# Kernel tuning notes

Hardware: AMD Instinct MI355X
Metric: run time of the kernel (lower is better)

## Reference

```python
import jax, jax.numpy as jnp
import numpy as np
from jax import lax

B, C, H, W = 4, 64, 128, 128
G, K, CO = 8, 3, 64
KK = K * K
MC = G * KK  # mask channels = 72


def _conv3x3(x, w, b):
    # standard 3x3 conv, stride 1, padding 1, NCHW
    y = lax.conv_general_dilated(x, w, (1, 1), ((1, 1), (1, 1)),
                                 dimension_numbers=('NCHW', 'OIHW', 'NCHW'))
    return y + b[None, :, None, None]


def _deform_conv2d(x, offset, mask, w, b):
    """Modulated deformable conv (DCNv2), stride=1, padding=1, dilation=1.
    offset: [B, 2*G*KK, H, W] interpreted as [B, G, KK, 2(dy,dx), H, W] (torchvision layout).
    mask:   [B, G*KK, H, W].
    w: [Co, C/G, K, K], b: [Co].
    """
    Bn, Cn, Hn, Wn = x.shape
    Co, Cg, Kh, Kw = w.shape
    Gn = Cn // Cg
    KKn = Kh * Kw
    Ho, Wo = Hn, Wn  # stride 1, pad 1, k 3

    off = offset.reshape(Bn, Gn, KKn, 2, Ho, Wo)
    dy, dx = off[:, :, :, 0], off[:, :, :, 1]
    m = mask.reshape(Bn, Gn, 1, KKn, Ho, Wo)

    kh = (jnp.arange(KKn) // Kw).astype(x.dtype)  # kernel row index
    kw = (jnp.arange(KKn) % Kw).astype(x.dtype)
    hh = jnp.arange(Ho, dtype=x.dtype)
    ww = jnp.arange(Wo, dtype=x.dtype)
    # sampling positions: h - pad + kh*dil + dy  -> [B,G,KK,Ho,Wo]
    py = hh[None, None, None, :, None] - 1.0 + kh[None, None, :, None, None] + dy
    px = ww[None, None, None, None, :] - 1.0 + kw[None, None, :, None, None] + dx

    y0 = jnp.floor(py); x0 = jnp.floor(px)
    ly = py - y0; lx = px - x0
    y0i = y0.astype(jnp.int32); x0i = x0.astype(jnp.int32)
    y1i = y0i + 1; x1i = x0i + 1

    xg = x.reshape(Bn, Gn, Cg, Hn * Wn)

    def corner(yi, xi, wgt):
        valid = ((yi >= 0) & (yi < Hn) & (xi >= 0) & (xi < Wn)).astype(x.dtype)
        idx = (jnp.clip(yi, 0, Hn - 1) * Wn + jnp.clip(xi, 0, Wn - 1))
        idx = idx.reshape(Bn, Gn, 1, KKn * Ho * Wo)
        v = jnp.take_along_axis(xg, idx, axis=3).reshape(Bn, Gn, Cg, KKn, Ho, Wo)
        return v * (wgt * valid)[:, :, None]

    val = (corner(y0i, x0i, (1.0 - ly) * (1.0 - lx))
           + corner(y0i, x1i, (1.0 - ly) * lx)
           + corner(y1i, x0i, ly * (1.0 - lx))
           + corner(y1i, x1i, ly * lx))
    val = val * m  # modulation

    wr = w.reshape(Gn, Co // Gn, Cg, KKn)
    out = jnp.einsum('bgckhw,gock->bgohw', val, wr).reshape(Bn, Co, Ho, Wo)
    return out + b[None, :, None, None]


def setup_inputs() -> dict:
    key = jax.random.key(0)
    ks = jax.random.split(key, 8)
    f = lambda k, s, sc=1.0: jax.random.normal(k, s, dtype=jnp.float32) * sc
    return {
        'x': f(ks[0], (B, C, H, W)),
        'share_with_feat': f(ks[1], (B, C, H, W)),
        'offset_feat': f(ks[2], (B, C, H, W)),
        # conv_offset_mask: C -> 3*G*KK (zero-init in original; small random here)
        'w_om': f(ks[3], (3 * MC, C, 3, 3), 0.02),
        'b_om': jnp.zeros((3 * MC,), jnp.float32),
        'w_em1': f(ks[4], (C, 2 * C, 3, 3), 0.05),
        'b_em1': jnp.zeros((C,), jnp.float32),
        'w_em2': f(ks[5], (MC, C, 3, 3), 0.05),
        'b_em2': jnp.zeros((MC,), jnp.float32),
        # deform conv weight: [Co, C/G, 3, 3]
        'w_dc': f(ks[6], (CO, C // G, 3, 3), 0.05),
        'b_dc': f(ks[7], (CO,), 0.05),
    }


def reference(x, share_with_feat, offset_feat, w_om, b_om, w_em1, b_em1,
              w_em2, b_em2, w_dc, b_dc):
    om = _conv3x3(offset_feat, w_om, b_om)
    o1, o2, mask_x = jnp.split(om, 3, axis=1)
    offset = jnp.concatenate([o1, o2], axis=1)
    mask_x = jax.nn.sigmoid(mask_x)
    x_deform = _deform_conv2d(x, offset, mask_x, w_dc, b_dc)
    # extra_mask=True branch
    em = _conv3x3(jnp.concatenate([share_with_feat, offset_feat], axis=1), w_em1, b_em1)
    em = jnp.where(em >= 0, em, 0.1 * em)  # LeakyReLU(0.1)
    em = jax.nn.sigmoid(_conv3x3(em, w_em2, b_em2))
    share_deform = _deform_conv2d(share_with_feat, offset, em, w_dc, b_dc)
    return (x_deform, share_deform)
```

## Files before the change

### kernel.cpp

```cpp
#include <hip/hip_runtime.h>
#include <math.h>

#define BB 4
#define CC 64
#define HH 128
#define WW 128
#define GG 8
#define COO 64
#define HWC (HH*WW)

#define DPAD 12
#define DROW 26

typedef float f32x16 __attribute__((ext_vector_type(16)));
typedef __bf16 bf16x8 __attribute__((ext_vector_type(8)));

__device__ __forceinline__ unsigned short bf16_rn(float f) {
    unsigned int u = __float_as_uint(f);
    unsigned int r = (u + 0x7fffu + ((u >> 16) & 1u)) >> 16;
    return (unsigned short)r;
}
__device__ __forceinline__ float b2f(unsigned short u) {
    return __uint_as_float(((unsigned int)u) << 16);
}

__global__ __launch_bounds__(256) void pack_inputs_kernel(
    const float* __restrict__ x, const float* __restrict__ share,
    const float* __restrict__ offf,
    unsigned int* __restrict__ xs, unsigned short* __restrict__ sc16,
    unsigned short* __restrict__ oc16)
{
    __shared__ unsigned short lds[64][66];
    const int b = blockIdx.y;
    const int pix0 = blockIdx.x * 64;
    const int t = threadIdx.x;
    const int p = t & 63, q = t >> 6;
    const int pl = t & 63, cg = t >> 6;

#pragma unroll
    for (int i = 0; i < 16; i++) {
        int c = i * 4 + q;
        size_t idx = ((size_t)b * 64 + c) * HWC + pix0 + p;
        unsigned short sb = bf16_rn(share[idx]);
        lds[c][p] = sb;
        xs[idx] = (unsigned int)bf16_rn(x[idx]) | ((unsigned int)sb << 16);
    }
    __syncthreads();
    {
        unsigned int u[8];
#pragma unroll
        for (int j = 0; j < 8; j++) {
            unsigned int lo = lds[cg * 16 + 2 * j][pl];
            unsigned int hi = lds[cg * 16 + 2 * j + 1][pl];
            u[j] = lo | (hi << 16);
        }
        unsigned int* dst = (unsigned int*)(sc16 + ((size_t)(b * 4 + cg) * HWC + pix0 + pl) * 16);
        *(uint4*)dst = make_uint4(u[0], u[1], u[2], u[3]);
        *(uint4*)(dst + 4) = make_uint4(u[4], u[5], u[6], u[7]);
    }
    __syncthreads();

#pragma unroll
    for (int i = 0; i < 16; i++) {
        int c = i * 4 + q;
        lds[c][p] = bf16_rn(offf[((size_t)b * 64 + c) * HWC + pix0 + p]);
    }
    __syncthreads();
    {
        unsigned int u[8];
#pragma unroll
        for (int j = 0; j < 8; j++) {
            unsigned int lo = lds[cg * 16 + 2 * j][pl];
            unsigned int hi = lds[cg * 16 + 2 * j + 1][pl];
            u[j] = lo | (hi << 16);
        }
        unsigned int* dst = (unsigned int*)(oc16 + ((size_t)(b * 4 + cg) * HWC + pix0 + pl) * 16);
        *(uint4*)dst = make_uint4(u[0], u[1], u[2], u[3]);
        *(uint4*)(dst + 4) = make_uint4(u[4], u[5], u[6], u[7]);
    }
}

__device__ __forceinline__ void pack_w_one(const float* __restrict__ w,
                                           unsigned short* __restrict__ wp,
                                           int Cout, int COP, int CinTot, int idx) {
    int i  = idx & 15;
    int co = (idx >> 4) % COP;
    int t  = idx / (16 * COP);
    int cg = t & 3;
    int kk = (t >> 2) % 9;
    int seg = t / 36;
    int cin = seg * 64 + cg * 16 + i;
    float v = (co < Cout) ? w[((size_t)co * CinTot + cin) * 9 + kk] : 0.f;
    wp[idx] = bf16_rn(v);
}

__global__ void pack_w_all_kernel(const float* __restrict__ w_om, unsigned short* __restrict__ wp_om,
                                  const float* __restrict__ w_em1, unsigned short* __restrict__ wp_em1,
                                  const float* __restrict__ w_em2, unsigned short* __restrict__ wp_em2) {
    int i = blockIdx.x * 256 + threadIdx.x;
    if (i < 129024) {
        pack_w_one(w_om, wp_om, 216, 224, 64, i);
    } else if (i < 129024 + 73728) {
        pack_w_one(w_em1, wp_em1, 64, 64, 128, i - 129024);
    } else if (i < 129024 + 73728 + 55296) {
        pack_w_one(w_em2, wp_em2, 72, 96, 64, i - 129024 - 73728);
    }
}

template<int NSEG, int NT>
__global__ __launch_bounds__(256) void conv_mfma_kernel(
    const unsigned short* __restrict__ in0,
    const unsigned short* __restrict__ in1,
    const unsigned short* __restrict__ wp,
    const float* __restrict__ bias,
    void* __restrict__ out,
    int Cout, int COP, int out_mode, int act)
{
    constexpr int XS = 128 / (NT * 32);
    const int lane = threadIdx.x & 63;
    const int wid  = threadIdx.x >> 6;
    const int l31  = lane & 31;
    const int half = lane >> 5;
    int tmp = blockIdx.x;
    const int xsp = tmp % XS; tmp /= XS;
    const int rb  = tmp % (HH / 4);
    const int b   = tmp / (HH / 4);
    const int r   = rb * 4 + wid;
    const int px0 = xsp * NT * 32;
    const int co0 = blockIdx.y * 32;

    f32x16 acc[NT];
#pragma unroll
    for (int nt = 0; nt < NT; nt++)
#pragma unroll
        for (int rg = 0; rg < 16; rg++) acc[nt][rg] = 0.f;

    bf16x8 bz;
#pragma unroll
    for (int i = 0; i < 8; i++) bz[i] = (__bf16)0.f;

#pragma unroll
    for (int seg = 0; seg < NSEG; seg++) {
        const unsigned short* in = seg ? in1 : in0;
        const unsigned short* inb = in + (size_t)b * 4 * HWC * 16;
#pragma unroll
        for (int kk = 0; kk < 9; kk++) {
            const int rr = r + kk / 3 - 1;
            const bool rv = (unsigned)rr < (unsigned)HH;
            const int rrc = min(max(rr, 0), HH - 1);
            const int dxo = kk % 3 - 1;
#pragma unroll
            for (int cg = 0; cg < 4; cg++) {
                bf16x8 afrag = *(const bf16x8*)(wp +
                    ((size_t)(((seg * 9 + kk) * 4 + cg) * COP + co0 + l31) * 16 + half * 8));
                if (!rv) afrag = bz;
                const size_t plane = ((size_t)cg * HWC + (size_t)rrc * WW) * 16;
#pragma unroll
                for (int nt = 0; nt < NT; nt++) {
                    const int cc = px0 + nt * 32 + l31 + dxo;
                    bf16x8 bfrag = bz;
                    if ((unsigned)cc < (unsigned)WW)
                        bfrag = *(const bf16x8*)(inb + plane + (size_t)cc * 16 + half * 8);
                    acc[nt] = __builtin_amdgcn_mfma_f32_32x32x16_bf16(afrag, bfrag, acc[nt], 0, 0, 0);
                }
            }
        }
    }

#pragma unroll
    for (int nt = 0; nt < NT; nt++) {
#pragma unroll
        for (int rg = 0; rg < 16; rg++) {
            const int row = (rg & 3) + 8 * (rg >> 2) + 4 * half;
            const int co = co0 + row;
            if (co < Cout) {
                float v = acc[nt][rg] + bias[co];
                if (act == 1)      v = (v >= 0.f) ? v : 0.1f * v;
                else if (act == 2) v = 1.f / (1.f + __expf(-v));
                else if (act == 3 && co >= 144) v = 1.f / (1.f + __expf(-v));
                const int pix = r * WW + px0 + nt * 32 + l31;
                if (out_mode == 2)
                    ((unsigned short*)out)[((size_t)b * Cout + co) * HWC + pix] = bf16_rn(v);
                else
                    ((unsigned short*)out)[((size_t)(b * 4 + (co >> 4)) * HWC + pix) * 16 + (co & 15)] = bf16_rn(v);
            }
        }
    }
}

__global__ __launch_bounds__(256) void deform_fused_kernel(
    const unsigned int* __restrict__ xs,
    const unsigned short* __restrict__ om, const unsigned short* __restrict__ em,
    const float* __restrict__ wdc, const float* __restrict__ bdc,
    float* __restrict__ outx, float* __restrict__ outs)
{
    __shared__ __align__(16) unsigned int lds[24 * DROW * DPAD];

    const int bg = blockIdx.x >> 6;
    const int b = bg >> 3, g = bg & 7;
    const int tile = blockIdx.x & 63;
    const int r0 = (tile >> 3) << 4;
    const int c0 = (tile & 7) << 4;
    const int tx = threadIdx.x & 15, ty = threadIdx.x >> 4;
    const int h = r0 + ty, w = c0 + tx;
    const int wr0 = r0 - 4, wc0 = c0 - 4;

    const unsigned int* xsb = xs + ((size_t)b * 64 + g * 8) * HWC;

#pragma unroll
    for (int i = 0; i < 18; i++) {
        unsigned int slot = (unsigned int)threadIdx.x + i * 256u;
        unsigned int sx = slot % 24u;
        unsigned int t2 = slot / 24u;
        unsigned int sy = t2 % 24u;
        unsigned int c  = t2 / 24u;
        int iy = min(max(wr0 + (int)sy, 0), HH - 1);
        int ix = min(max(wc0 + (int)sx, 0), WW - 1);
        lds[(sy * DROW + sx) * DPAD + c] = xsb[(size_t)c * HWC + iy * WW + ix];
    }

    __syncthreads();

    const int pix = h * WW + w;
    const unsigned short* omb = om + (size_t)b * 216 * HWC + pix + (size_t)g * 18 * HWC;
    const unsigned short* mmb = om + (size_t)b * 216 * HWC + pix + (size_t)(144 + g * 9) * HWC;
    const unsigned short* emb = em + (size_t)b * 72 * HWC + pix + (size_t)g * 9 * HWC;

    float accx[8], accs[8];
#pragma unroll
    for (int o = 0; o < 8; o++) { accx[o] = 0.f; accs[o] = 0.f; }

#pragma unroll
    for (int kk = 0; kk < 9; kk++) {
        const float dy = b2f(omb[(size_t)(kk * 2) * HWC]);
        const float dx = b2f(omb[(size_t)(kk * 2 + 1) * HWC]);
        const float m1 = b2f(mmb[(size_t)kk * HWC]);
        const float m2 = b2f(emb[(size_t)kk * HWC]);

        const float py = (float)(h - 1 + kk / 3) + dy;
        const float px = (float)(w - 1 + kk % 3) + dx;
        const float y0f = floorf(py), x0f = floorf(px);
        const float ly = py - y0f, lx = px - x0f;
        const int y0 = (int)y0f, x0 = (int)x0f;
        const int y1 = y0 + 1, x1 = x0 + 1;
        const bool vy0 = (y0 >= 0) && (y0 < HH), vy1 = (y1 >= 0) && (y1 < HH);
        const bool vx0 = (x0 >= 0) && (x0 < WW), vx1 = (x1 >= 0) && (x1 < WW);
        float w00 = (1.f - ly) * (1.f - lx); if (!(vy0 && vx0)) w00 = 0.f;
        float w01 = (1.f - ly) * lx;         if (!(vy0 && vx1)) w01 = 0.f;
        float w10 = ly * (1.f - lx);         if (!(vy1 && vx0)) w10 = 0.f;
        float w11 = ly * lx;                 if (!(vy1 && vx1)) w11 = 0.f;
        const int cy0 = min(max(y0, 0), HH - 1), cy1 = min(max(y1, 0), HH - 1);
        const int cx0 = min(max(x0, 0), WW - 1), cx1 = min(max(x1, 0), WW - 1);

        const int sy0 = cy0 - wr0, sy1 = cy1 - wr0;
        const int sx0 = cx0 - wc0, sx1 = cx1 - wc0;
        const bool inw = (sy0 >= 0) && (sy1 < 24) && (sx0 >= 0) && (sx1 < 24);

        const float* wk = wdc + (size_t)g * 8 * 8 * 9 + kk;

        if (__builtin_expect(inw, 1)) {
            const int p00 = (sy0 * DROW + sx0) * DPAD, p01 = (sy0 * DROW + sx1) * DPAD;
            const int p10 = (sy1 * DROW + sx0) * DPAD, p11 = (sy1 * DROW + sx1) * DPAD;
#pragma unroll
            for (int ch = 0; ch < 2; ch++) {
                uint4 qa = *(const uint4*)(lds + p00 + ch * 4);
                uint4 qb = *(const uint4*)(lds + p01 + ch * 4);
                uint4 qc = *(const uint4*)(lds + p10 + ch * 4);
                uint4 qd = *(const uint4*)(lds + p11 + ch * 4);
                const unsigned int ua[4] = {qa.x, qa.y, qa.z, qa.w};
                const unsigned int ub[4] = {qb.x, qb.y, qb.z, qb.w};
                const unsigned int uc[4] = {qc.x, qc.y, qc.z, qc.w};
                const unsigned int ud[4] = {qd.x, qd.y, qd.z, qd.w};
#pragma unroll
                for (int j = 0; j < 4; j++) {
                    const int c = ch * 4 + j;
                    float x00 = __uint_as_float(ua[j] << 16), s00 = __uint_as_float(ua[j] & 0xffff0000u);
                    float x01 = __uint_as_float(ub[j] << 16), s01 = __uint_as_float(ub[j] & 0xffff0000u);
                    float x10 = __uint_as_float(uc[j] << 16), s10 = __uint_as_float(uc[j] & 0xffff0000u);
                    float x11 = __uint_as_float(ud[j] << 16), s11 = __uint_as_float(ud[j] & 0xffff0000u);
                    float vx = w00 * x00; vx = fmaf(w01, x01, vx); vx = fmaf(w10, x10, vx); vx = fmaf(w11, x11, vx);
                    float vs = w00 * s00; vs = fmaf(w01, s01, vs); vs = fmaf(w10, s10, vs); vs = fmaf(w11, s11, vs);
                    vx *= m1;
                    vs *= m2;
#pragma unroll
                    for (int o = 0; o < 8; o++) {
                        const float wv = wk[(size_t)(o * 8 + c) * 9];
                        accx[o] = fmaf(vx, wv, accx[o]);
                        accs[o] = fmaf(vs, wv, accs[o]);
                    }
                }
            }
        } else {
            const int i00 = cy0 * WW + cx0, i01 = cy0 * WW + cx1;
            const int i10 = cy1 * WW + cx0, i11 = cy1 * WW + cx1;
#pragma unroll
            for (int c = 0; c < 8; c++) {
                const unsigned int* xc = xsb + (size_t)c * HWC;
                unsigned int a = xc[i00], bq = xc[i01], cq = xc[i10], dq = xc[i11];
                float x00 = __uint_as_float(a << 16),  s00 = __uint_as_float(a & 0xffff0000u);
                float x01 = __uint_as_float(bq << 16), s01 = __uint_as_float(bq & 0xffff0000u);
                float x10 = __uint_as_float(cq << 16), s10 = __uint_as_float(cq & 0xffff0000u);
                float x11 = __uint_as_float(dq << 16), s11 = __uint_as_float(dq & 0xffff0000u);
                float vx = w00 * x00; vx = fmaf(w01, x01, vx); vx = fmaf(w10, x10, vx); vx = fmaf(w11, x11, vx);
                float vs = w00 * s00; vs = fmaf(w01, s01, vs); vs = fmaf(w10, s10, vs); vs = fmaf(w11, s11, vs);
                vx *= m1;
                vs *= m2;
#pragma unroll
                for (int o = 0; o < 8; o++) {
                    const float wv = wk[(size_t)(o * 8 + c) * 9];
                    accx[o] = fmaf(vx, wv, accx[o]);
                    accs[o] = fmaf(vs, wv, accs[o]);
                }
            }
        }
    }

#pragma unroll
    for (int o = 0; o < 8; o++) {
        const float bv = bdc[g * 8 + o];
        outx[((size_t)(b * COO + g * 8 + o)) * HWC + pix] = accx[o] + bv;
        outs[((size_t)(b * COO + g * 8 + o)) * HWC + pix] = accs[o] + bv;
    }
}

extern "C" void kernel_launch(void* const* d_in, const int* in_sizes, int n_in,
                              void* d_out, int out_size, void* d_ws, size_t ws_size,
                              hipStream_t stream) {
    const float* x      = (const float*)d_in[0];
    const float* share  = (const float*)d_in[1];
    const float* offf   = (const float*)d_in[2];
    const float* w_om   = (const float*)d_in[3];
    const float* b_om   = (const float*)d_in[4];
    const float* w_em1  = (const float*)d_in[5];
    const float* b_em1  = (const float*)d_in[6];
    const float* w_em2  = (const float*)d_in[7];
    const float* b_em2  = (const float*)d_in[8];
    const float* w_dc   = (const float*)d_in[9];
    const float* b_dc   = (const float*)d_in[10];

    unsigned int* xs = (unsigned int*)d_ws;
    unsigned short* us = (unsigned short*)(xs + 4194304);
    unsigned short* sc16   = us;
    unsigned short* oc16   = sc16 + 4194304;
    unsigned short* emm    = oc16 + 4194304;
    unsigned short* om_b   = emm + 4194304;
    unsigned short* em_b   = om_b + 14155776;
    unsigned short* wp_om  = em_b + 4718592;
    unsigned short* wp_em1 = wp_om + 129024;
    unsigned short* wp_em2 = wp_em1 + 73728;

    float* outx = (float*)d_out;
    float* outs = outx + 4194304;

    dim3 blk(256);

    pack_inputs_kernel<<<dim3(HWC / 64, BB), blk, 0, stream>>>(x, share, offf, xs, sc16, oc16);
    pack_w_all_kernel<<<(258048 + 255) / 256, blk, 0, stream>>>(
        w_om, wp_om, w_em1, wp_em1, w_em2, wp_em2);

    conv_mfma_kernel<1, 2><<<dim3(BB * (HH / 4) * 2, 7), blk, 0, stream>>>(
        oc16, nullptr, wp_om, b_om, om_b, 216, 224, 2, 3);
    conv_mfma_kernel<2, 1><<<dim3(BB * (HH / 4) * 4, 2), blk, 0, stream>>>(
        sc16, oc16, wp_em1, b_em1, emm, 64, 64, 3, 1);
    conv_mfma_kernel<1, 1><<<dim3(BB * (HH / 4) * 4, 3), blk, 0, stream>>>(
        emm, nullptr, wp_em2, b_em2, em_b, 72, 96, 2, 2);

    deform_fused_kernel<<<dim3(BB * GG * 64), blk, 0, stream>>>(
        xs, om_b, em_b, w_dc, b_dc, outx, outs);
}
```

Before: 276.6 us.

## Stage conv input halo tiles in LDS and tile multiple output-channel blocks per wave

The MFMA 3x3 conv kernel now cooperatively loads a 4-row-plus-halo, 66-pixel input tile for all channel groups into shared memory, then reads B fragments from LDS for every kernel tap, where before each fragment came from global memory. Each wave also computes MREP 32-channel output blocks, so every B fragment feeds several MFMAs. Weight packing pads the output channels to 256/128 to match the new blocking. This cuts redundant global loads of the input, in exchange for extra padded work on the om/em2 convs, shared-memory use, and a barrier between segments.

```diff
diff --git a/kernel.cpp b/kernel.cpp
--- a/kernel.cpp
+++ b/kernel.cpp
@@ -98,91 +98,118 @@
                                   const float* __restrict__ w_em1, unsigned short* __restrict__ wp_em1,
                                   const float* __restrict__ w_em2, unsigned short* __restrict__ wp_em2) {
     int i = blockIdx.x * 256 + threadIdx.x;
-    if (i < 129024) {
-        pack_w_one(w_om, wp_om, 216, 224, 64, i);
-    } else if (i < 129024 + 73728) {
-        pack_w_one(w_em1, wp_em1, 64, 64, 128, i - 129024);
-    } else if (i < 129024 + 73728 + 55296) {
-        pack_w_one(w_em2, wp_em2, 72, 96, 64, i - 129024 - 73728);
-    }
-}
-
-template<int NSEG, int NT>
+    if (i < 147456) {
+        pack_w_one(w_om, wp_om, 216, 256, 64, i);
+    } else if (i < 147456 + 73728) {
+        pack_w_one(w_em1, wp_em1, 64, 64, 128, i - 147456);
+    } else if (i < 147456 + 73728 + 73728) {
+        pack_w_one(w_em2, wp_em2, 72, 128, 64, i - 147456 - 73728);
+    }
+}
+
+template<int NSEG, int MREP, int COP>
 __global__ __launch_bounds__(256) void conv_mfma_kernel(
     const unsigned short* __restrict__ in0,
     const unsigned short* __restrict__ in1,
     const unsigned short* __restrict__ wp,
     const float* __restrict__ bias,
     void* __restrict__ out,
-    int Cout, int COP, int out_mode, int act)
+    int Cout, int out_mode, int act)
 {
-    constexpr int XS = 128 / (NT * 32);
+    constexpr int NT  = 2;
+    constexpr int PXW = NT * 32 + 2;
+    constexpr int NE  = 4 * 6 * PXW;
+    __shared__ __align__(16) unsigned short slds[NE * 16];
+
     const int lane = threadIdx.x & 63;
     const int wid  = threadIdx.x >> 6;
     const int l31  = lane & 31;
     const int half = lane >> 5;
     int tmp = blockIdx.x;
-    const int xsp = tmp % XS; tmp /= XS;
-    const int rb  = tmp % (HH / 4);
-    const int b   = tmp / (HH / 4);
-    const int r   = rb * 4 + wid;
-    const int px0 = xsp * NT * 32;
-    const int co0 = blockIdx.y * 32;
-
-    f32x16 acc[NT];
-#pragma unroll
-    for (int nt = 0; nt < NT; nt++)
-#pragma unroll
-        for (int rg = 0; rg < 16; rg++) acc[nt][rg] = 0.f;
-
-    bf16x8 bz;
-#pragma unroll
-    for (int i = 0; i < 8; i++) bz[i] = (__bf16)0.f;
-
-#pragma unroll
+    const int xsp = tmp & 1; tmp >>= 1;
+    const int rb  = tmp & 31;
+    const int b   = tmp >> 5;
+    const int r0  = rb * 4;
+    const int r   = r0 + wid;
+    const int px0 = xsp * 64;
+    const int co0 = blockIdx.y * (32 * MREP);
+
+    f32x16 acc[MREP][NT];
+#pragma unroll
+    for (int m = 0; m < MREP; m++)
+#pragma unroll
+        for (int nt = 0; nt < NT; nt++)
+#pragma unroll
+            for (int rg = 0; rg < 16; rg++) acc[m][nt][rg] = 0.f;
+
+    const int lbase = (wid * PXW + l31) * 16 + half * 8;
+
     for (int seg = 0; seg < NSEG; seg++) {
-        const unsigned short* in = seg ? in1 : in0;
-        const unsigned short* inb = in + (size_t)b * 4 * HWC * 16;
+        const unsigned short* inb = (seg ? in1 : in0) + (size_t)b * 4 * HWC * 16;
+        if (seg) __syncthreads();
+
+        for (int e = threadIdx.x; e < NE; e += 256) {
+            const int cg  = e / (6 * PXW);
+            const int rem = e - cg * (6 * PXW);
+            const int row = rem / PXW;
+            const int px  = rem - row * PXW;
+            const int iy = r0 - 1 + row;
+            const int ix = px0 - 1 + px;
+            const bool valid = ((unsigned)iy < (unsigned)HH) && ((unsigned)ix < (unsigned)WW);
+            const int iyc = min(max(iy, 0), HH - 1);
+            const int ixc = min(max(ix, 0), WW - 1);
+            const uint4* src = (const uint4*)(inb + ((size_t)cg * HWC + (size_t)iyc * WW + ixc) * 16);
+            uint4 v0, v1;
+            if (valid) { v0 = src[0]; v1 = src[1]; }
+            else       { v0 = make_uint4(0u, 0u, 0u, 0u); v1 = v0; }
+            uint4* dst = (uint4*)(slds + (size_t)e * 16);
+            dst[0] = v0; dst[1] = v1;
+        }
+        __syncthreads();
+
 #pragma unroll
         for (int kk = 0; kk < 9; kk++) {
-            const int rr = r + kk / 3 - 1;
-            const bool rv = (unsigned)rr < (unsigned)HH;
-            const int rrc = min(max(rr, 0), HH - 1);
-            const int dxo = kk % 3 - 1;
+            const int kh = kk / 3, kw = kk % 3;
 #pragma unroll
             for (int cg = 0; cg < 4; cg++) {
-                bf16x8 afrag = *(const bf16x8*)(wp +
-                    ((size_t)(((seg * 9 + kk) * 4 + cg) * COP + co0 + l31) * 16 + half * 8));
-                if (!rv) afrag = bz;
-                const size_t plane = ((size_t)cg * HWC + (size_t)rrc * WW) * 16;
+                const int t = (seg * 9 + kk) * 4 + cg;
+                bf16x8 af[MREP];
+#pragma unroll
+                for (int m = 0; m < MREP; m++)
+                    af[m] = *(const bf16x8*)(wp +
+                        (size_t)(t * COP + co0 + m * 32 + l31) * 16 + half * 8);
 #pragma unroll
                 for (int nt = 0; nt < NT; nt++) {
-                    const int cc = px0 + nt * 32 + l31 + dxo;
-                    bf16x8 bfrag = bz;
-                    if ((unsigned)cc < (unsigned)WW)
-                        bfrag = *(const bf16x8*)(inb + plane + (size_t)cc * 16 + half * 8);
-                    acc[nt] = __builtin_amdgcn_mfma_f32_32x32x16_bf16(afrag, bfrag, acc[nt], 0, 0, 0);
+                    const bf16x8 bf = *(const bf16x8*)(slds + lbase +
+                        ((cg * 6 + kh) * PXW + nt * 32 + kw) * 16);
+#pragma unroll
+                    for (int m = 0; m < MREP; m++)
+                        acc[m][nt] = __builtin_amdgcn_mfma_f32_32x32x16_bf16(
+                            af[m], bf, acc[m][nt], 0, 0, 0);
                 }
             }
         }
     }
 
 #pragma unroll
-    for (int nt = 0; nt < NT; nt++) {
-#pragma unroll
-        for (int rg = 0; rg < 16; rg++) {
-            const int row = (rg & 3) + 8 * (rg >> 2) + 4 * half;
-            const int co = co0 + row;
-            if (co < Cout) {
-                float v = acc[nt][rg] + bias[co];
-                if (act == 1)      v = (v >= 0.f) ? v : 0.1f * v;
-                else if (act == 2) v = 1.f / (1.f + __expf(-v));
-                else if (act == 3 && co >= 144) v = 1.f / (1.f + __expf(-v));
-                const int pix = r * WW + px0 + nt * 32 + l31;
-                if (out_mode == 2)
-                    ((unsigned short*)out)[((size_t)b * Cout + co) * HWC + pix] = bf16_rn(v);
-                else
-                    ((unsigned short*)out)[((size_t)(b * 4 + (co >> 4)) * HWC + pix) * 16 + (co & 15)] = bf16_rn(v);
+    for (int m = 0; m < MREP; m++) {
+#pragma unroll
+        for (int nt = 0; nt < NT; nt++) {
+#pragma unroll
+            for (int rg = 0; rg < 16; rg++) {
+                const int row = (rg & 3) + 8 * (rg >> 2) + 4 * half;
+                const int co = co0 + m * 32 + row;
+                if (co < Cout) {
+                    float v = acc[m][nt][rg] + bias[co];
+                    if (act == 1)      v = (v >= 0.f) ? v : 0.1f * v;
+                    else if (act == 2) v = 1.f / (1.f + __expf(-v));
+                    else if (act == 3 && co >= 144) v = 1.f / (1.f + __expf(-v));
+                    const int pix = r * WW + px0 + nt * 32 + l31;
+                    if (out_mode == 2)
+                        ((unsigned short*)out)[((size_t)b * Cout + co) * HWC + pix] = bf16_rn(v);
+                    else
+                        ((unsigned short*)out)[((size_t)(b * 4 + (co >> 4)) * HWC + pix) * 16 + (co & 15)] = bf16_rn(v);
+                }
             }
         }
     }
@@ -346,7 +373,7 @@
     unsigned short* om_b   = emm + 4194304;
     unsigned short* em_b   = om_b + 14155776;
     unsigned short* wp_om  = em_b + 4718592;
-    unsigned short* wp_em1 = wp_om + 129024;
+    unsigned short* wp_em1 = wp_om + 147456;
     unsigned short* wp_em2 = wp_em1 + 73728;
 
     float* outx = (float*)d_out;
@@ -355,15 +382,15 @@
     dim3 blk(256);
 
     pack_inputs_kernel<<<dim3(HWC / 64, BB), blk, 0, stream>>>(x, share, offf, xs, sc16, oc16);
-    pack_w_all_kernel<<<(258048 + 255) / 256, blk, 0, stream>>>(
+    pack_w_all_kernel<<<(147456 + 73728 + 73728) / 256, blk, 0, stream>>>(
         w_om, wp_om, w_em1, wp_em1, w_em2, wp_em2);
 
-    conv_mfma_kernel<1, 2><<<dim3(BB * (HH / 4) * 2, 7), blk, 0, stream>>>(
-        oc16, nullptr, wp_om, b_om, om_b, 216, 224, 2, 3);
-    conv_mfma_kernel<2, 1><<<dim3(BB * (HH / 4) * 4, 2), blk, 0, stream>>>(
-        sc16, oc16, wp_em1, b_em1, emm, 64, 64, 3, 1);
-    conv_mfma_kernel<1, 1><<<dim3(BB * (HH / 4) * 4, 3), blk, 0, stream>>>(
-        emm, nullptr, wp_em2, b_em2, em_b, 72, 96, 2, 2);
+    conv_mfma_kernel<1, 2, 256><<<dim3(256, 4), blk, 0, stream>>>(
+        oc16, nullptr, wp_om, b_om, om_b, 216, 2, 3);
+    conv_mfma_kernel<2, 1, 64><<<dim3(256, 2), blk, 0, stream>>>(
+        sc16, oc16, wp_em1, b_em1, emm, 64, 3, 1);
+    conv_mfma_kernel<1, 2, 128><<<dim3(256, 2), blk, 0, stream>>>(
+        emm, nullptr, wp_em2, b_em2, em_b, 72, 2, 2);
 
     deform_fused_kernel<<<dim3(BB * GG * 64), blk, 0, stream>>>(
         xs, om_b, em_b, w_dc, b_dc, outx, outs);
```

Result: slower. 296.9 us (+7.3%).
